# Optimization experiments

Hardware: AMD Instinct MI355X
Metric: run time of the kernel (lower is better)

The kernel has to match this reference:

```python
import jax, jax.numpy as jnp
import numpy as np

PAGE_SIZE = 16
NUM_PAGES = 256
H = 32          # query heads
HKV = 8         # kv heads
D = 128         # head dim
HIDDEN = 4096
SEQ = 2048
ROPE_THETA = 10000.0


def _rope(x, pos):
    # x: [S, h, D], pos: [S]; non-interleaved (rotate-half) RoPE as in
    # flashinfer.rope.apply_rope_pos_ids_inplace / HF Llama.
    half = x.shape[-1] // 2
    inv_freq = 1.0 / (ROPE_THETA ** (jnp.arange(half, dtype=jnp.float32) / half))
    ang = pos.astype(jnp.float32)[:, None] * inv_freq          # [S, half]
    cos = jnp.cos(ang)[:, None, :]
    sin = jnp.sin(ang)[:, None, :]
    x1, x2 = x[..., :half], x[..., half:]
    return jnp.concatenate([x1 * cos - x2 * sin, x2 * cos + x1 * sin], axis=-1).astype(x.dtype)


def setup_inputs() -> dict:
    key = jax.random.key(0)
    ks = jax.random.split(key, 6)
    return {
        "hidden_states": jax.random.normal(ks[0], (1, SEQ, HIDDEN), jnp.float32),
        "position_ids": jnp.arange(SEQ, dtype=jnp.int32),
        "page_indices": jnp.arange(SEQ // PAGE_SIZE, dtype=jnp.int32),  # 128 distinct pages
        "Wq": jax.random.normal(ks[1], (H * D, HIDDEN), jnp.float32) * 0.02,
        "Wk": jax.random.normal(ks[2], (HKV * D, HIDDEN), jnp.float32) * 0.02,
        "Wv": jax.random.normal(ks[3], (HKV * D, HIDDEN), jnp.float32) * 0.02,
        "Wo": jax.random.normal(ks[4], (HIDDEN, H * D), jnp.float32) * 0.02,
        "kv_cache": jnp.zeros((NUM_PAGES, 2, PAGE_SIZE, HKV, D), jnp.float32),
    }


def reference(hidden_states, position_ids, page_indices, Wq, Wk, Wv, Wo, kv_cache):
    S = hidden_states.shape[1]
    x = hidden_states[0]                                  # [S, HIDDEN] (module squeezes batch=1)
    q = (x @ Wq.T).reshape(S, H, D)
    k = (x @ Wk.T).reshape(S, HKV, D)
    v = (x @ Wv.T).reshape(S, HKV, D)
    q = _rope(q, position_ids)
    k = _rope(k, position_ids)

    # Write K/V into the paged cache (page_table.write_block per page)
    n_used = page_indices.shape[0]
    k_pages = k.reshape(n_used, PAGE_SIZE, HKV, D)
    v_pages = v.reshape(n_used, PAGE_SIZE, HKV, D)
    cache = kv_cache.at[page_indices, 0].set(k_pages).at[page_indices, 1].set(v_pages)

    # Gather paged KV back for attention (BatchPrefillWithPagedKVCache)
    kk = cache[page_indices, 0].reshape(-1, HKV, D)[:S]   # [S, HKV, D]
    vv = cache[page_indices, 1].reshape(-1, HKV, D)[:S]

    # GQA: expand kv heads to query heads
    group = H // HKV
    k_rep = jnp.repeat(kk, group, axis=1)                 # [S, H, D]
    v_rep = jnp.repeat(vv, group, axis=1)

    scale = D ** -0.5
    scores = jnp.einsum('qhd,khd->hqk', q * scale, k_rep)  # [H, S, S]
    causal = jnp.arange(S)[:, None] >= jnp.arange(S)[None, :]
    scores = jnp.where(causal[None], scores, jnp.finfo(scores.dtype).min)
    probs = jax.nn.softmax(scores, axis=-1)
    attn = jnp.einsum('hqk,khd->qhd', probs, v_rep)        # [S, H, D]

    out = attn.reshape(S, H * D) @ Wo.T                    # o_proj
    return out[None]                                       # [1, S, HIDDEN]
```

## Files before the change

### kernel.cpp

```cpp
#include <hip/hip_runtime.h>
#include <hip/hip_bf16.h>
#include <math.h>

#define SEQ    2048
#define HIDDEN 4096
#define NH     32
#define NKV    8
#define HD     128
#define QKV_N  6144

typedef __attribute__((ext_vector_type(8))) short bf16x8;
typedef __attribute__((ext_vector_type(4))) float f32x4;
typedef unsigned short u16;
typedef unsigned int u32;

__device__ inline void gl_lds16(const void* g, void* lds) {
  __builtin_amdgcn_global_load_lds((const __attribute__((address_space(1))) void*)g,
                                   (__attribute__((address_space(3))) void*)lds, 16, 0, 0);
}

__device__ inline u16 f2bf(float f) {
  __hip_bfloat16 h = __float2bfloat16(f);
  return *(u16*)&h;
}
__device__ inline float bf2f(u16 u) {
  __hip_bfloat16 h = *(__hip_bfloat16*)&u;
  return __bfloat162float(h);
}

__global__ void cvt_f32_bf16(const float* __restrict__ src, u16* __restrict__ dst, int n8) {
  int i = blockIdx.x * blockDim.x + threadIdx.x;
  if (i >= n8) return;
  const float4* s = (const float4*)src + (size_t)i * 2;
  float4 a = s[0], b = s[1];
  float v[8] = {a.x, a.y, a.z, a.w, b.x, b.y, b.z, b.w};
  union { u16 o[8]; uint4 u; } pk;
#pragma unroll
  for (int j = 0; j < 8; j++) pk.o[j] = f2bf(v[j]);
  *(uint4*)(dst + (size_t)i * 8) = pk.u;
}

template <int OUTF32>
__global__ __launch_bounds__(256) void gemm_bt(const u16* __restrict__ A,
                                               const u16* __restrict__ B,
                                               void* __restrict__ Cout,
                                               int M, int N, int K) {
  __shared__ __align__(16) u16 As[128 * 32];
  __shared__ __align__(16) u16 Bs[128 * 32];
  const int tid = threadIdx.x;
  const int wave = tid >> 6, lane = tid & 63;
  const int quad = lane >> 4, l16 = lane & 15;
  const int wm = wave >> 1, wn = wave & 1;
  const int m0 = blockIdx.y * 128, n0 = blockIdx.x * 128;

  f32x4 acc[4][4] = {};
  const int lrow = lane >> 2;
  const int kchunk = (lane & 3) * 8;

  for (int k0 = 0; k0 < K; k0 += 32) {
    __syncthreads();
#pragma unroll
    for (int i = 0; i < 2; i++) {
      int r = wave * 32 + i * 16 + lrow;
      gl_lds16(A + (size_t)(m0 + r) * K + k0 + kchunk, &As[(wave * 32 + i * 16) * 32]);
      gl_lds16(B + (size_t)(n0 + r) * K + k0 + kchunk, &Bs[(wave * 32 + i * 16) * 32]);
    }
    __syncthreads();
    bf16x8 af[4], bfr[4];
#pragma unroll
    for (int t = 0; t < 4; t++) {
      af[t]  = *(const bf16x8*)&As[(wm * 64 + t * 16 + l16) * 32 + quad * 8];
      bfr[t] = *(const bf16x8*)&Bs[(wn * 64 + t * 16 + l16) * 32 + quad * 8];
    }
#pragma unroll
    for (int mt = 0; mt < 4; mt++)
#pragma unroll
      for (int nt = 0; nt < 4; nt++)
        acc[mt][nt] = __builtin_amdgcn_mfma_f32_16x16x32_bf16(af[mt], bfr[nt], acc[mt][nt], 0, 0, 0);
  }

#pragma unroll
  for (int mt = 0; mt < 4; mt++)
#pragma unroll
    for (int nt = 0; nt < 4; nt++)
#pragma unroll
      for (int r = 0; r < 4; r++) {
        int row = m0 + wm * 64 + mt * 16 + quad * 4 + r;
        int col = n0 + wn * 64 + nt * 16 + l16;
        float v = acc[mt][nt][r];
        if (OUTF32) ((float*)Cout)[(size_t)row * N + col] = v;
        else        ((u16*)Cout)[(size_t)row * N + col] = f2bf(v);
      }
}

__global__ void rope_kernel(u16* __restrict__ qkv, const int* __restrict__ pos_ids) {
  int idx = blockIdx.x * blockDim.x + threadIdx.x;
  int d = idx & 63;
  int h = (idx >> 6) % 40;
  int s = idx / (64 * 40);
  if (s >= SEQ) return;
  int off = (h < NH) ? h * HD : HIDDEN + (h - NH) * HD;
  u16* base = qkv + (size_t)s * QKV_N + off;
  float inv_freq = powf(10000.0f, -(float)d * (1.0f / 64.0f));
  float ang = (float)pos_ids[s] * inv_freq;
  float sn, cs;
  sincosf(ang, &sn, &cs);
  float x1 = bf2f(base[d]);
  float x2 = bf2f(base[d + 64]);
  base[d]      = f2bf(x1 * cs - x2 * sn);
  base[d + 64] = f2bf(x2 * cs + x1 * sn);
}

__global__ __launch_bounds__(256) void transpose_v(const u16* __restrict__ qkv,
                                                   u16* __restrict__ vt) {
  __shared__ u16 t[64][72];
  const int s0 = blockIdx.x * 64, c0 = blockIdx.y * 64;
  const int tid = threadIdx.x;
#pragma unroll
  for (int i = 0; i < 2; i++) {
    int r = (tid >> 3) + i * 32;
    int c = (tid & 7) * 8;
    *(uint4*)&t[r][c] = *(const uint4*)&qkv[(size_t)(s0 + r) * QKV_N + 5120 + c0 + c];
  }
  __syncthreads();
#pragma unroll
  for (int i = 0; i < 2; i++) {
    int c = (tid >> 3) + i * 32;
    int s = (tid & 7) * 8;
    union { uint4 u; u16 e[8]; } o;
#pragma unroll
    for (int j = 0; j < 8; j++) o.e[j] = t[s + j][c];
    *(uint4*)&vt[(size_t)(c0 + c) * SEQ + s0 + s] = o.u;
  }
}

__global__ __launch_bounds__(128, 3) void attn_kernel(const u16* __restrict__ qkv,
                                                      const u16* __restrict__ vt,
                                                      u16* __restrict__ attn_out) {
  __shared__ __align__(16) float Ex[32 * 132];
  const int blk = blockIdx.x;
  const int kvh = blk & 7;
  const int hg = (blk >> 3) & 3;
  const int it = 63 - (blk >> 5);
  const int h  = kvh * 4 + hg;
  const int tid = threadIdx.x;
  const int wave = tid >> 6, lane = tid & 63;
  const int quad = lane >> 4, l16 = lane & 15;
  const int q0 = it * 32;

  const float c = 0.08838834764831845f * 1.4426950408889634f;

  bf16x8 qf[2][4];
#pragma unroll
  for (int m = 0; m < 2; m++)
#pragma unroll
    for (int dc = 0; dc < 4; dc++)
      qf[m][dc] = *(const bf16x8*)(qkv + (size_t)(q0 + m * 16 + l16) * QKV_N + h * HD + dc * 32 + quad * 8);

  const u16* kp[4];
#pragma unroll
  for (int st = 0; st < 4; st++)
    kp[st] = qkv + (size_t)(wave * 64 + st * 16 + l16) * QKV_N + HIDDEN + kvh * HD + quad * 8;
  const u16* vp[8];
#pragma unroll
  for (int dt = 0; dt < 8; dt++)
    vp[dt] = vt + (size_t)(kvh * HD + dt * 16 + l16) * SEQ + wave * 64 + quad * 8;

  float lsum[2] = {0.f, 0.f};
  f32x4 o[2][8] = {};

  const int srcA = ((lane >> 4) & 1) * 32 + l16;
  const int srcB = srcA + 16;
  const bool hi = quad >= 2;

  const int n_kt = (q0 + 95) >> 6;
  for (int kt = wave; kt < n_kt; kt += 2) {
    const bool last = (kt == n_kt - 1);

    u32 pk[2][4][2];
#pragma unroll
    for (int st = 0; st < 4; st++) {
      bf16x8 kst[4];
#pragma unroll
      for (int dc = 0; dc < 4; dc++) kst[dc] = *(const bf16x8*)(kp[st] + dc * 32);
      f32x4 s[2] = {};
#pragma unroll
      for (int dc = 0; dc < 4; dc++)
#pragma unroll
        for (int m = 0; m < 2; m++)
          s[m] = __builtin_amdgcn_mfma_f32_16x16x32_bf16(kst[dc], qf[m][dc], s[m], 0, 0, 0);
#pragma unroll
      for (int m = 0; m < 2; m++) {
        float pr[4];
#pragma unroll
        for (int r = 0; r < 4; r++) {
          float v = fmaf(s[m][r], c, -32.0f);
          if (last) {
            int key = kt * 64 + st * 16 + quad * 4 + r;
            if (key > q0 + m * 16 + l16) v = -1e30f;
          }
          pr[r] = exp2f(v);
          lsum[m] += pr[r];
        }
        pk[m][st][0] = ((u32)f2bf(pr[1]) << 16) | f2bf(pr[0]);
        pk[m][st][1] = ((u32)f2bf(pr[3]) << 16) | f2bf(pr[2]);
      }
    }

    bf16x8 pf[2][2];
#pragma unroll
    for (int m = 0; m < 2; m++)
#pragma unroll
      for (int kc = 0; kc < 2; kc++) {
        union { u32 w[4]; bf16x8 v; } u;
        u32 a0 = (u32)__shfl((int)pk[m][2 * kc][0],     srcA);
        u32 b0 = (u32)__shfl((int)pk[m][2 * kc + 1][0], srcA);
        u32 a1 = (u32)__shfl((int)pk[m][2 * kc][1],     srcA);
        u32 b1 = (u32)__shfl((int)pk[m][2 * kc + 1][1], srcA);
        u32 a2 = (u32)__shfl((int)pk[m][2 * kc][0],     srcB);
        u32 b2 = (u32)__shfl((int)pk[m][2 * kc + 1][0], srcB);
        u32 a3 = (u32)__shfl((int)pk[m][2 * kc][1],     srcB);
        u32 b3 = (u32)__shfl((int)pk[m][2 * kc + 1][1], srcB);
        u.w[0] = hi ? b0 : a0;
        u.w[1] = hi ? b1 : a1;
        u.w[2] = hi ? b2 : a2;
        u.w[3] = hi ? b3 : a3;
        pf[m][kc] = u.v;
      }

#pragma unroll
    for (int dt = 0; dt < 8; dt++) {
      bf16x8 vf0 = *(const bf16x8*)(vp[dt]);
      bf16x8 vf1 = *(const bf16x8*)(vp[dt] + 32);
#pragma unroll
      for (int m = 0; m < 2; m++) {
        o[m][dt] = __builtin_amdgcn_mfma_f32_16x16x32_bf16(vf0, pf[m][0], o[m][dt], 0, 0, 0);
        o[m][dt] = __builtin_amdgcn_mfma_f32_16x16x32_bf16(vf1, pf[m][1], o[m][dt], 0, 0, 0);
      }
    }

#pragma unroll
    for (int st = 0; st < 4; st++) kp[st] += (size_t)128 * QKV_N;
#pragma unroll
    for (int dt = 0; dt < 8; dt++) vp[dt] += 128;
  }

#pragma unroll
  for (int m = 0; m < 2; m++) {
    lsum[m] += __shfl_xor(lsum[m], 16);
    lsum[m] += __shfl_xor(lsum[m], 32);
  }

  if (wave == 1) {
#pragma unroll
    for (int m = 0; m < 2; m++) {
#pragma unroll
      for (int dt = 0; dt < 8; dt++)
        *(f32x4*)&Ex[(m * 16 + l16) * 132 + dt * 16 + quad * 4] = o[m][dt];
      if (lane < 16) Ex[(m * 16 + l16) * 132 + 128] = lsum[m];
    }
  }
  __syncthreads();
  if (wave == 0) {
#pragma unroll
    for (int m = 0; m < 2; m++) {
      float lt = lsum[m] + Ex[(m * 16 + l16) * 132 + 128];
      float inv = 1.0f / lt;
      size_t base = (size_t)(q0 + m * 16 + l16) * HIDDEN + h * HD;
#pragma unroll
      for (int dt = 0; dt < 8; dt++) {
        f32x4 p = *(const f32x4*)&Ex[(m * 16 + l16) * 132 + dt * 16 + quad * 4];
        float v0 = (o[m][dt][0] + p[0]) * inv;
        float v1 = (o[m][dt][1] + p[1]) * inv;
        float v2 = (o[m][dt][2] + p[2]) * inv;
        float v3 = (o[m][dt][3] + p[3]) * inv;
        u32 w0 = ((u32)f2bf(v1) << 16) | f2bf(v0);
        u32 w1 = ((u32)f2bf(v3) << 16) | f2bf(v2);
        uint2 wv; wv.x = w0; wv.y = w1;
        *(uint2*)&attn_out[base + dt * 16 + quad * 4] = wv;
      }
    }
  }
}

extern "C" void kernel_launch(void* const* d_in, const int* in_sizes, int n_in,
                              void* d_out, int out_size, void* d_ws, size_t ws_size,
                              hipStream_t stream) {
  const float* x  = (const float*)d_in[0];
  const int* pos  = (const int*)d_in[1];
  const float* Wq = (const float*)d_in[3];
  const float* Wk = (const float*)d_in[4];
  const float* Wv = (const float*)d_in[5];
  const float* Wo = (const float*)d_in[6];
  float* out = (float*)d_out;

  u16* x_bf    = (u16*)d_ws;
  u16* Wqkv_bf = x_bf + (size_t)SEQ * HIDDEN;
  u16* qkv_bf  = Wqkv_bf + (size_t)QKV_N * HIDDEN;
  u16* attn_bf = qkv_bf + (size_t)SEQ * QKV_N;
  u16* Wo_bf   = attn_bf + (size_t)SEQ * HIDDEN;
  u16* vt_bf   = x_bf;

  auto cvt = [&](const float* s, u16* d, size_t n) {
    int n8 = (int)(n / 8);
    cvt_f32_bf16<<<(n8 + 255) / 256, 256, 0, stream>>>(s, d, n8);
  };
  cvt(x,  x_bf,    (size_t)SEQ * HIDDEN);
  cvt(Wq, Wqkv_bf,                         (size_t)4096 * 4096);
  cvt(Wk, Wqkv_bf + (size_t)4096 * 4096,   (size_t)1024 * 4096);
  cvt(Wv, Wqkv_bf + (size_t)5120 * 4096,   (size_t)1024 * 4096);
  cvt(Wo, Wo_bf,   (size_t)4096 * 4096);

  dim3 g1(QKV_N / 128, SEQ / 128);
  gemm_bt<0><<<g1, 256, 0, stream>>>(x_bf, Wqkv_bf, qkv_bf, SEQ, QKV_N, HIDDEN);

  int rope_threads = SEQ * 40 * 64;
  rope_kernel<<<rope_threads / 256, 256, 0, stream>>>(qkv_bf, pos);

  dim3 gt(SEQ / 64, 1024 / 64);
  transpose_v<<<gt, 256, 0, stream>>>(qkv_bf, vt_bf);

  attn_kernel<<<2048, 128, 0, stream>>>(qkv_bf, vt_bf, attn_bf);

  dim3 g3(HIDDEN / 128, SEQ / 128);
  gemm_bt<1><<<g3, 256, 0, stream>>>(attn_bf, Wo_bf, out, SEQ, HIDDEN, HIDDEN);
}
```

Measured before the change: 639.3 us.

## Rewrite GEMMs with 256-row tiles, 4-stage LDS pipeline, swizzle and XCD remap

Replaces the 128x128 single-buffered bf16 GEMM with a 512-thread kernel using 256xBN tiles and a 4-deep ring of LDS buffers. Global-to-LDS loads are issued three tiles ahead and gated with explicit vmcnt waits, so the barrier-wait-compute serialization is removed. The kernel also adds an XOR swizzle on LDS columns to avoid bank conflicts, raises wave priority around the MFMA block, and remaps block IDs so adjacent tiles land on the same XCD for L2 reuse. In exchange it uses much more LDS and more accumulator registers, and the O-projection grid has only 256 blocks, which may underfill the GPU.

```diff
diff --git a/kernel.cpp b/kernel.cpp
--- a/kernel.cpp
+++ b/kernel.cpp
@@ -14,9 +14,17 @@
 typedef unsigned short u16;
 typedef unsigned int u32;
 
+#define VMCNT(n) asm volatile("s_waitcnt vmcnt(" #n ")" ::: "memory")
+
 __device__ inline void gl_lds16(const void* g, void* lds) {
   __builtin_amdgcn_global_load_lds((const __attribute__((address_space(1))) void*)g,
                                    (__attribute__((address_space(3))) void*)lds, 16, 0, 0);
+}
+
+__device__ inline void tile_barrier() {
+  __builtin_amdgcn_sched_barrier(0);
+  __builtin_amdgcn_s_barrier();
+  __builtin_amdgcn_sched_barrier(0);
 }
 
 __device__ inline u16 f2bf(float f) {
@@ -40,54 +48,95 @@
   *(uint4*)(dst + (size_t)i * 8) = pk.u;
 }
 
-template <int OUTF32>
-__global__ __launch_bounds__(256) void gemm_bt(const u16* __restrict__ A,
-                                               const u16* __restrict__ B,
-                                               void* __restrict__ Cout,
-                                               int M, int N, int K) {
-  __shared__ __align__(16) u16 As[128 * 32];
-  __shared__ __align__(16) u16 Bs[128 * 32];
+template <int OUTF32, int NF>
+__global__ __launch_bounds__(512, 2) void gemm_bt2(const u16* __restrict__ A,
+                                                   const u16* __restrict__ B,
+                                                   void* __restrict__ Cout,
+                                                   int M, int N, int K) {
+  __shared__ __align__(16) u16 Abuf[4][256 * 32];
+  __shared__ __align__(16) u16 Bbuf[4][NF * 64 * 32];
   const int tid = threadIdx.x;
-  const int wave = tid >> 6, lane = tid & 63;
+  const int w = tid >> 6, lane = tid & 63;
   const int quad = lane >> 4, l16 = lane & 15;
-  const int wm = wave >> 1, wn = wave & 1;
-  const int m0 = blockIdx.y * 128, n0 = blockIdx.x * 128;
-
-  f32x4 acc[4][4] = {};
-  const int lrow = lane >> 2;
-  const int kchunk = (lane & 3) * 8;
-
-  for (int k0 = 0; k0 < K; k0 += 32) {
-    __syncthreads();
-#pragma unroll
-    for (int i = 0; i < 2; i++) {
-      int r = wave * 32 + i * 16 + lrow;
-      gl_lds16(A + (size_t)(m0 + r) * K + k0 + kchunk, &As[(wave * 32 + i * 16) * 32]);
-      gl_lds16(B + (size_t)(n0 + r) * K + k0 + kchunk, &Bs[(wave * 32 + i * 16) * 32]);
-    }
-    __syncthreads();
-    bf16x8 af[4], bfr[4];
-#pragma unroll
-    for (int t = 0; t < 4; t++) {
-      af[t]  = *(const bf16x8*)&As[(wm * 64 + t * 16 + l16) * 32 + quad * 8];
-      bfr[t] = *(const bf16x8*)&Bs[(wn * 64 + t * 16 + l16) * 32 + quad * 8];
-    }
-#pragma unroll
-    for (int mt = 0; mt < 4; mt++)
-#pragma unroll
-      for (int nt = 0; nt < 4; nt++)
-        acc[mt][nt] = __builtin_amdgcn_mfma_f32_16x16x32_bf16(af[mt], bfr[nt], acc[mt][nt], 0, 0, 0);
-  }
-
-#pragma unroll
-  for (int mt = 0; mt < 4; mt++)
-#pragma unroll
-    for (int nt = 0; nt < 4; nt++)
-#pragma unroll
-      for (int r = 0; r < 4; r++) {
-        int row = m0 + wm * 64 + mt * 16 + quad * 4 + r;
-        int col = n0 + wn * 64 + nt * 16 + l16;
-        float v = acc[mt][nt][r];
+  const int wm = w >> 2, wn = w & 3;
+  constexpr int BN = NF * 64;
+
+  const int nwg = gridDim.x;
+  const int bid = blockIdx.x;
+  const int qq = nwg >> 3, rr8 = nwg & 7;
+  const int xcd = bid & 7, loc = bid >> 3;
+  const int wg = (xcd < rr8 ? xcd * (qq + 1) : rr8 * (qq + 1) + (xcd - rr8) * qq) + loc;
+  const int nbx = N / BN;
+  const int m0 = (wg / nbx) * 256;
+  const int n0 = (wg % nbx) * BN;
+
+  const int srow = lane >> 2;
+  const int sswz = ((lane >> 2) & 3) ^ ((lane >> 4) & 1);
+  const int scol = ((lane & 3) ^ sswz) << 3;
+  const u16* aG = A + (size_t)(m0 + w * 16 + srow) * K + scol;
+  const u16* bG = B + (size_t)(n0 + w * 16 + srow) * K + scol;
+  const int NT = K >> 5;
+
+  const int swzr = (l16 & 3) ^ ((l16 >> 2) & 1);
+  const int kslot = (quad ^ swzr) << 3;
+
+  f32x4 acc[8][NF] = {};
+
+  auto stage = [&](int t) {
+    const int b = t & 3;
+    const size_t k0 = (size_t)t << 5;
+    gl_lds16(aG + k0,                   &Abuf[b][(w * 16) * 32]);
+    gl_lds16(aG + k0 + (size_t)128 * K, &Abuf[b][(128 + w * 16) * 32]);
+    gl_lds16(bG + k0,                   &Bbuf[b][(w * 16) * 32]);
+    if constexpr (NF == 4)
+      gl_lds16(bG + k0 + (size_t)128 * K, &Bbuf[b][(128 + w * 16) * 32]);
+  };
+
+  stage(0); stage(1); stage(2);
+  if constexpr (NF == 4) { VMCNT(8); } else { VMCNT(6); }
+  tile_barrier();
+
+  for (int t = 0; t < NT; ++t) {
+    const int b = t & 3;
+    if (t + 3 < NT) stage(t + 3);
+
+    bf16x8 af[8], bfr[NF];
+#pragma unroll
+    for (int f = 0; f < 8; ++f)
+      af[f] = *(const bf16x8*)&Abuf[b][(wm * 128 + f * 16 + l16) * 32 + kslot];
+#pragma unroll
+    for (int nf = 0; nf < NF; ++nf)
+      bfr[nf] = *(const bf16x8*)&Bbuf[b][(wn * (NF * 16) + nf * 16 + l16) * 32 + kslot];
+
+    __builtin_amdgcn_s_setprio(1);
+#pragma unroll
+    for (int f = 0; f < 8; ++f)
+#pragma unroll
+      for (int nf = 0; nf < NF; ++nf)
+        acc[f][nf] = __builtin_amdgcn_mfma_f32_16x16x32_bf16(af[f], bfr[nf], acc[f][nf], 0, 0, 0);
+    __builtin_amdgcn_s_setprio(0);
+
+    if (t < NT - 1) {
+      if (t + 3 < NT) {
+        if constexpr (NF == 4) { VMCNT(8); } else { VMCNT(6); }
+      } else if (t + 3 == NT) {
+        if constexpr (NF == 4) { VMCNT(4); } else { VMCNT(3); }
+      } else {
+        VMCNT(0);
+      }
+      tile_barrier();
+    }
+  }
+
+#pragma unroll
+  for (int f = 0; f < 8; ++f)
+#pragma unroll
+    for (int nf = 0; nf < NF; ++nf)
+#pragma unroll
+      for (int r = 0; r < 4; ++r) {
+        int row = m0 + wm * 128 + f * 16 + quad * 4 + r;
+        int col = n0 + wn * (NF * 16) + nf * 16 + l16;
+        float v = acc[f][nf][r];
         if (OUTF32) ((float*)Cout)[(size_t)row * N + col] = v;
         else        ((u16*)Cout)[(size_t)row * N + col] = f2bf(v);
       }
@@ -311,8 +360,8 @@
   cvt(Wv, Wqkv_bf + (size_t)5120 * 4096,   (size_t)1024 * 4096);
   cvt(Wo, Wo_bf,   (size_t)4096 * 4096);
 
-  dim3 g1(QKV_N / 128, SEQ / 128);
-  gemm_bt<0><<<g1, 256, 0, stream>>>(x_bf, Wqkv_bf, qkv_bf, SEQ, QKV_N, HIDDEN);
+  gemm_bt2<0, 4><<<dim3((SEQ / 256) * (QKV_N / 256)), 512, 0, stream>>>(
+      x_bf, Wqkv_bf, qkv_bf, SEQ, QKV_N, HIDDEN);
 
   int rope_threads = SEQ * 40 * 64;
   rope_kernel<<<rope_threads / 256, 256, 0, stream>>>(qkv_bf, pos);
@@ -322,6 +371,6 @@
 
   attn_kernel<<<2048, 128, 0, stream>>>(qkv_bf, vt_bf, attn_bf);
 
-  dim3 g3(HIDDEN / 128, SEQ / 128);
-  gemm_bt<1><<<g3, 256, 0, stream>>>(attn_bf, Wo_bf, out, SEQ, HIDDEN, HIDDEN);
-}
+  gemm_bt2<1, 2><<<dim3((SEQ / 256) * (HIDDEN / 128)), 512, 0, stream>>>(
+      attn_bf, Wo_bf, out, SEQ, HIDDEN, HIDDEN);
+}
```

Result: slower. 700.2 us (+9.5%).
